# Optimization experiments

Measured on AMD Instinct MI355X. Metric: run time of the kernel, lower is better.

## Reference

```python
import jax, jax.numpy as jnp
import numpy as np
from jax import lax

# Module config (UOT_loss defaults): reg_m_l2=[5.0, 5.0], div='l2',
# detach_plan=True, use_uniform=False, marginal_match_dim=1.
REG_M1, REG_M2 = 5.0, 5.0
NUM_ITER = 1000      # POT mm_unbalanced default numItermax
STOP_THR = 1e-15     # POT default stopThr
EPS = 1e-16


def pairwise_sqeuclidean(x, y):
    # ot.dist default metric='sqeuclidean': M[i,j] = ||x_i - y_j||^2
    x2 = jnp.sum(x * x, axis=1)[:, None]
    y2 = jnp.sum(y * y, axis=1)[None, :]
    return jnp.maximum(x2 + y2 - 2.0 * (x @ y.T), 0.0)


def mm_unbalanced_l2(a, b, M):
    # POT ot.unbalanced.mm_unbalanced(a, b, M, [REG_M1, REG_M2], div='l2'), reg=0.
    G0 = a[:, None] * b[None, :]                       # [n, m] init plan
    K = jnp.maximum(REG_M1 * a[:, None] + REG_M2 * b[None, :] - M, 0.0)

    def cond(state):
        i, _, err = state
        return jnp.logical_and(i < NUM_ITER, err > STOP_THR)

    def body(state):
        i, G, _ = state
        Gd = (REG_M1 * jnp.sum(G, axis=1, keepdims=True)
              + REG_M2 * jnp.sum(G, axis=0, keepdims=True) + EPS)
        Gn = K * G / Gd
        err = jnp.sqrt(jnp.sum((Gn - G) ** 2))
        return i + 1, Gn, err

    _, G, _ = lax.while_loop(
        cond, body, (jnp.int32(0), G0, jnp.array(jnp.inf, G0.dtype)))
    return G


def setup_inputs() -> dict:
    key = jax.random.key(0)
    k1, k2, k3, k4 = jax.random.split(key, 4)
    n, m, d = 4096, 4096, 64
    source = jax.random.normal(k1, (n, d), jnp.float32)
    target = jax.random.normal(k2, (m, d), jnp.float32)
    mu = jax.random.uniform(k3, (n,), jnp.float32, minval=0.5, maxval=1.5)
    nu = jax.random.uniform(k4, (m,), jnp.float32, minval=0.5, maxval=1.5)
    mu = mu / jnp.sum(mu)
    nu = nu / jnp.sum(nu)
    return {"source": source, "target": target,
            "source_density": mu, "target_density": nu}


def reference(source, target, source_density, target_density):
    M = pairwise_sqeuclidean(source, target)           # [n, m]
    plan = mm_unbalanced_l2(source_density, target_density, M)
    ot_loss = jnp.sum(plan * M)
    # marginal_match_dim=1 -> row sums (transported source mass)
    marginal_transported = jnp.sum(plan, axis=1)
    marginal_loss = jnp.mean((marginal_transported - source_density) ** 2)
    return ot_loss, marginal_loss
```

## Files before the change

kernel.cpp:

```cpp
#include <hip/hip_runtime.h>


#define NV 4096
#define RM 5.0f
#define EPSF 1e-16f
#define STOP2 1e-30f
#define NITER 1000
#define MAGIC 0x5a17c0de
#define GRID_T 512
#define NT 4096

#define ERRT_OFF 0
#define ERRS_OFF 4096
#define OTP_OFF  8192
#define RSP_OFF  12288
#define CSP_OFF  274432
#define RS_OFF   536576
#define CS_OFF   540672
#define BMI_OFF  544768
#define CTL_OFF  548864
#define G_OFF    552960

typedef short bf16x8 __attribute__((ext_vector_type(8)));
typedef float f32x4  __attribute__((ext_vector_type(4)));
typedef unsigned short u16;

__device__ __forceinline__ float wave_sum_all(float v) {
  #pragma unroll
  for (int off = 1; off < 64; off <<= 1) v += __shfl_xor(v, off);
  return v;
}
__device__ __forceinline__ float red32_sum(float v) {
  #pragma unroll
  for (int off = 1; off < 32; off <<= 1) v += __shfl_xor(v, off);
  return v;
}
__device__ __forceinline__ float red32_max(float v) {
  #pragma unroll
  for (int off = 1; off < 32; off <<= 1) v = fmaxf(v, __shfl_xor(v, off));
  return v;
}
__device__ __forceinline__ float wave_sum_dn(float v) {
  #pragma unroll
  for (int off = 32; off; off >>= 1) v += __shfl_down(v, off);
  return v;
}
__device__ __forceinline__ float dot64(const float* __restrict__ xr,
                                       const float* __restrict__ yr) {
  float d = 0.f;
  #pragma unroll 1
  for (int k = 0; k < 64; ++k) d = fmaf(xr[k], yr[k], d);
  return d;
}
__device__ __forceinline__ unsigned pack2(float x, float y) {
  return (__float_as_uint(x) >> 16) | (__float_as_uint(y) & 0xffff0000u);
}

__device__ void stage64(const float* __restrict__ X,
                        const float* __restrict__ Y,
                        int by, int bx,
                        u16 (*As)[72], u16 (*Bs)[72],
                        float* X2L, float* Y2L) {
  const int t = threadIdx.x;
  #pragma unroll
  for (int m = 0; m < 2; ++m) {
    const float* src = m ? (Y + (size_t)bx * 4096) : (X + (size_t)by * 4096);
    u16 (*dst)[72] = m ? Bs : As;
    float* nrm = m ? Y2L : X2L;
    #pragma unroll
    for (int it = 0; it < 4; ++it) {
      const int flat = t + it * 256;
      const int r = flat >> 4;
      const int c = (flat & 15) << 2;
      const float4 v = *(const float4*)(src + (size_t)flat * 4);
      float p = fmaf(v.x, v.x, fmaf(v.y, v.y, fmaf(v.z, v.z, v.w * v.w)));
      p += __shfl_xor(p, 1); p += __shfl_xor(p, 2);
      p += __shfl_xor(p, 4); p += __shfl_xor(p, 8);
      if ((t & 15) == 0) nrm[r] = p;
      uint2 w;
      w.x = pack2(v.x, v.y);
      w.y = pack2(v.z, v.w);
      *(uint2*)&dst[r][c] = w;
    }
  }
  __syncthreads();
}

__device__ void dots64(const u16 (*As)[72], const u16 (*Bs)[72],
                       int wr, int wc, int lane, f32x4 acc[2][2]) {
  const int lrow = lane & 15, lk8 = lane >> 4;
  #pragma unroll
  for (int i = 0; i < 2; ++i)
    #pragma unroll
    for (int j = 0; j < 2; ++j)
      acc[i][j] = (f32x4){0.f, 0.f, 0.f, 0.f};
  #pragma unroll
  for (int ks = 0; ks < 2; ++ks) {
    bf16x8 af[2], bg[2];
    #pragma unroll
    for (int f = 0; f < 2; ++f) {
      af[f] = *(const bf16x8*)&As[wr * 32 + f * 16 + lrow][ks * 32 + lk8 * 8];
      bg[f] = *(const bf16x8*)&Bs[wc * 32 + f * 16 + lrow][ks * 32 + lk8 * 8];
    }
    #pragma unroll
    for (int fr = 0; fr < 2; ++fr)
      #pragma unroll
      for (int fc = 0; fc < 2; ++fc)
        acc[fr][fc] = __builtin_amdgcn_mfma_f32_16x16x32_bf16(
            af[fr], bg[fc], acc[fr][fc], 0, 0, 0);
  }
}

__device__ __forceinline__ void gbar(int* ctl) {
  __threadfence();
  __syncthreads();
  if (threadIdx.x == 0) {
    while (__hip_atomic_load(&ctl[2], __ATOMIC_ACQUIRE,
                             __HIP_MEMORY_SCOPE_AGENT) != (int)MAGIC)
      __builtin_amdgcn_s_sleep(8);
    const int sense = __hip_atomic_load(&ctl[1], __ATOMIC_ACQUIRE,
                                        __HIP_MEMORY_SCOPE_AGENT);
    const int old = __hip_atomic_fetch_add(&ctl[0], 1, __ATOMIC_ACQ_REL,
                                           __HIP_MEMORY_SCOPE_AGENT);
    if (old == GRID_T - 1) {
      __hip_atomic_store(&ctl[0], 0, __ATOMIC_RELAXED, __HIP_MEMORY_SCOPE_AGENT);
      __hip_atomic_store(&ctl[1], sense ^ 1, __ATOMIC_RELEASE,
                         __HIP_MEMORY_SCOPE_AGENT);
    } else {
      while (__hip_atomic_load(&ctl[1], __ATOMIC_ACQUIRE,
                               __HIP_MEMORY_SCOPE_AGENT) == sense)
        __builtin_amdgcn_s_sleep(16);
    }
  }
  __syncthreads();
  __threadfence();
}

__global__ __launch_bounds__(256, 5) void k_main(
    const float* __restrict__ X, const float* __restrict__ Y,
    const float* __restrict__ a, const float* __restrict__ b,
    float* __restrict__ W) {
  __shared__ u16 As[64][72], Bs[64][72];
  __shared__ float X2L[64], Y2L[64];
  __shared__ float rcs[128];
  __shared__ float serr[4];
  __shared__ int s_nz;

  const int bid = blockIdx.x, tid = threadIdx.x;
  const int by = bid >> 6, bx = bid & 63;
  const int lane = tid & 63, wv = tid >> 6;
  const int wr = wv >> 1, wc = wv & 1;
  const int lrow = lane & 15, lk8 = lane >> 4;
  const int l32 = lane & 31;
  const int r0w = by * 64 + wr * 32, c0w = bx * 64 + wc * 32;
  float* Gp = W + G_OFF;
  int* bmi = (int*)(W + BMI_OFF);

  if (tid == 0) s_nz = 0;
  if (tid < 128) rcs[tid] = 0.f;

  stage64(X, Y, by, bx, As, Bs, X2L, Y2L);

  const float av = a[r0w + l32];
  const float bv = b[c0w + l32];

  f32x4 acc[2][2];
  dots64(As, Bs, wr, wc, lane, acc);

  const float x2lv = X2L[wr * 32 + l32];
  const float y2lv = Y2L[wc * 32 + l32];
  const float amax = red32_max(av), bmax = red32_max(bv);
  const float x2m = red32_max(x2lv), y2m = red32_max(y2lv);
  const float Cw = RM * (amax + bmax) + 0.02f * sqrtf(x2m * y2m) + 0.05f;

  float x2r[8], y2c[2];
  #pragma unroll
  for (int fr = 0; fr < 2; ++fr)
    #pragma unroll
    for (int j = 0; j < 4; ++j)
      x2r[fr * 4 + j] = X2L[wr * 32 + fr * 16 + lk8 * 4 + j];
  #pragma unroll
  for (int fc = 0; fc < 2; ++fc)
    y2c[fc] = Y2L[wc * 32 + fc * 16 + lrow];

  float mmin = 3.4e38f;
  #pragma unroll
  for (int fr = 0; fr < 2; ++fr)
    #pragma unroll
    for (int j = 0; j < 4; ++j)
      #pragma unroll
      for (int fc = 0; fc < 2; ++fc)
        mmin = fminf(mmin,
                     fmaf(-2.f, acc[fr][fc][j], x2r[fr * 4 + j] + y2c[fc]));
  const bool wfast = (__ballot(mmin < Cw) == 0ull);

  if (wfast) {
    const float Ea = red32_sum(av * av);
    const float Eb = red32_sum(bv * bv);
    if (lane == 0) serr[wv] = Ea * Eb;
    #pragma unroll
    for (int fr = 0; fr < 2; ++fr)
      #pragma unroll
      for (int fc = 0; fc < 2; ++fc)
        acc[fr][fc] = (f32x4){0.f, 0.f, 0.f, 0.f};
  } else {
    if (lane == 0) s_nz = 1;
    float sa = 0.f, sb = 0.f;
    for (int i = lane; i < NV; i += 64) { sa += a[i]; sb += b[i]; }
    sa = wave_sum_all(sa); sb = wave_sum_all(sb);
    float bcf[2], gdc[2];
    #pragma unroll
    for (int fc = 0; fc < 2; ++fc) {
      bcf[fc] = __shfl(bv, fc * 16 + lrow);
      gdc[fc] = RM * bcf[fc] * sa;
    }
    float errp = 0.f;
    #pragma unroll
    for (int fr = 0; fr < 2; ++fr)
      #pragma unroll
      for (int j = 0; j < 4; ++j) {
        const int ridx = fr * 16 + lk8 * 4 + j;
        const float ar = __shfl(av, ridx);
        const float gdr = RM * ar * sb;
        const int grow = r0w + ridx;
        float rsum = 0.f;
        #pragma unroll
        for (int fc = 0; fc < 2; ++fc) {
          float Mv = fmaf(-2.f, acc[fr][fc][j], x2r[fr * 4 + j] + y2c[fc]);
          if (Mv < Cw) {
            const float dx = dot64(X + ((size_t)grow << 6),
                                   Y + ((size_t)(c0w + fc * 16 + lrow) << 6));
            Mv = dot64(X + ((size_t)grow << 6), X + ((size_t)grow << 6)) * 0.f
               + x2r[fr * 4 + j] + y2c[fc] - 2.f * dx;
          }
          Mv = fmaxf(Mv, 0.f);
          const float Kv = fmaxf(RM * (ar + bcf[fc]) - Mv, 0.f);
          const float g0 = ar * bcf[fc];
          const float g = Kv * g0 / (gdr + gdc[fc] + EPSF);
          acc[fr][fc][j] = g;
          const float dl = g - g0;
          errp += dl * dl;
          rsum += g;
        }
        atomicAdd(&rcs[wr * 32 + ridx], rsum);
      }
    #pragma unroll
    for (int fc = 0; fc < 2; ++fc) {
      float csum = 0.f;
      #pragma unroll
      for (int fr = 0; fr < 2; ++fr)
        #pragma unroll
        for (int j = 0; j < 4; ++j) csum += acc[fr][fc][j];
      atomicAdd(&rcs[64 + wc * 32 + fc * 16 + lrow], csum);
    }
    errp = wave_sum_all(errp);
    if (lane == 0) serr[wv] = errp;
  }
  __syncthreads();
  const int tilenz = s_nz;

  if (tilenz) {
    #pragma unroll
    for (int fr = 0; fr < 2; ++fr)
      #pragma unroll
      for (int j = 0; j < 4; ++j) {
        const int grow = r0w + fr * 16 + lk8 * 4 + j;
        #pragma unroll
        for (int fc = 0; fc < 2; ++fc)
          Gp[(size_t)grow * NV + c0w + fc * 16 + lrow] = acc[fr][fc][j];
      }
    if (tid < 64)       W[RSP_OFF + (size_t)bid * 64 + tid] = rcs[tid];
    else if (tid < 128) W[CSP_OFF + (size_t)bid * 64 + (tid - 64)] = rcs[tid];
  }
  if (tid == 0) {
    W[ERRT_OFF + bid] = serr[0] + serr[1] + serr[2] + serr[3];
    bmi[bid] = tilenz;
  }
}

__global__ __launch_bounds__(256, 2) void k_tail(
    const float* __restrict__ X, const float* __restrict__ Y,
    const float* __restrict__ a, const float* __restrict__ b,
    float* __restrict__ W, float* __restrict__ out) {
  __shared__ u16 As[64][72], Bs[64][72];
  __shared__ float X2L[64], Y2L[64];
  __shared__ float rcs[128], serr[4], sred[4];
  __shared__ int s_nz, s_any;

  const int bid = blockIdx.x, tid = threadIdx.x;
  const int lane = tid & 63, wv = tid >> 6;
  const int wr = wv >> 1, wc = wv & 1;
  const int lrow = lane & 15, lk8 = lane >> 4;
  const int l32 = lane & 31;
  float* Gp = W + G_OFF;
  int* bmi = (int*)(W + BMI_OFF);
  int* ctl = (int*)(W + CTL_OFF);

  if (bid == 0 && tid == 0) {
    __hip_atomic_store(&ctl[0], 0, __ATOMIC_RELAXED, __HIP_MEMORY_SCOPE_AGENT);
    __hip_atomic_store(&ctl[1], 0, __ATOMIC_RELAXED, __HIP_MEMORY_SCOPE_AGENT);
    __hip_atomic_store(&ctl[2], (int)MAGIC, __ATOMIC_RELEASE,
                       __HIP_MEMORY_SCOPE_AGENT);
  }

  const int4* bmi4 = (const int4*)bmi;
  int orv = 0;
  for (int i = tid; i < 1024; i += 256) {
    const int4 q = bmi4[i];
    orv |= q.x | q.y | q.z | q.w;
  }
  if (tid == 0) s_any = 0;
  __syncthreads();
  if (orv) s_any = 1;
  __syncthreads();

  if (!s_any) {
    if (bid == 0) {
      float s = 0.f;
      for (int i = tid; i < NV; i += 256) { const float d = a[i]; s = fmaf(d, d, s); }
      s = wave_sum_dn(s);
      if (lane == 0) serr[wv] = s;
      __syncthreads();
      if (tid == 0) {
        out[0] = 0.f;
        out[1] = (serr[0] + serr[1] + serr[2] + serr[3]) * (1.0f / (float)NV);
      }
    }
    return;
  }

  int p = 2;
  while (true) {
    {
      const int sr = tid >> 5, j32 = tid & 31;
      const int r = bid * 8 + sr;
      const int byr = r >> 6, rl = r & 63;
      float vs = 0.f;
      for (int k = j32; k < 64; k += 32) {
        const int t = byr * 64 + k;
        vs += bmi[t] ? W[RSP_OFF + (size_t)t * 64 + rl] : 0.f;
      }
      vs = red32_sum(vs);
      if (j32 == 0) W[RS_OFF + r] = vs;
      float cs = 0.f;
      for (int k = j32; k < 64; k += 32) {
        const int t = k * 64 + byr;
        cs += bmi[t] ? W[CSP_OFF + (size_t)t * 64 + rl] : 0.f;
      }
      cs = red32_sum(cs);
      if (j32 == 0) W[CS_OFF + r] = cs;
    }
    if (bid == 0) {
      float e = 0.f;
      for (int i = tid; i < NT; i += 256) e += W[ERRT_OFF + i];
      e = wave_sum_all(e);
      if (lane == 0) sred[wv] = e;
      __syncthreads();
      if (tid == 0) W[ERRS_OFF] = sred[0] + sred[1] + sred[2] + sred[3];
    }
    gbar(ctl);
    const float errv = W[ERRS_OFF];
    if (errv <= STOP2 || p > NITER) break;

    #pragma unroll 1
    for (int tt = 0; tt < 8; ++tt) {
      const int t = bid + tt * GRID_T;
      if (!bmi[t]) { if (tid == 0) W[ERRT_OFF + t] = 0.f; continue; }
      const int by = t >> 6, bx = t & 63;
      const int r0w = by * 64 + wr * 32, c0w = bx * 64 + wc * 32;
      if (tid == 0) s_nz = 0;
      if (tid < 128) rcs[tid] = 0.f;
      __syncthreads();
      stage64(X, Y, by, bx, As, Bs, X2L, Y2L);
      f32x4 acc[2][2];
      dots64(As, Bs, wr, wc, lane, acc);

      const float av = a[r0w + l32], bv = b[c0w + l32];
      const float x2lv = X2L[wr * 32 + l32], y2lv = Y2L[wc * 32 + l32];
      const float Rv = W[RS_OFF + r0w + l32], Cv = W[CS_OFF + c0w + l32];
      const float amax = red32_max(av), bmax = red32_max(bv);
      const float x2m = red32_max(x2lv), y2m = red32_max(y2lv);
      const float Cw = RM * (amax + bmax) + 0.02f * sqrtf(x2m * y2m) + 0.05f;

      float x2r[8], y2c[2], bcf[2], Ccf[2];
      #pragma unroll
      for (int fr = 0; fr < 2; ++fr)
        #pragma unroll
        for (int j = 0; j < 4; ++j)
          x2r[fr * 4 + j] = X2L[wr * 32 + fr * 16 + lk8 * 4 + j];
      #pragma unroll
      for (int fc = 0; fc < 2; ++fc) {
        y2c[fc] = Y2L[wc * 32 + fc * 16 + lrow];
        bcf[fc] = __shfl(bv, fc * 16 + lrow);
        Ccf[fc] = __shfl(Cv, fc * 16 + lrow);
      }

      float errp = 0.f; int nzl = 0;
      #pragma unroll
      for (int fr = 0; fr < 2; ++fr)
        #pragma unroll
        for (int j = 0; j < 4; ++j) {
          const int ridx = fr * 16 + lk8 * 4 + j;
          const float ar = __shfl(av, ridx);
          const float Rr = __shfl(Rv, ridx);
          const int grow = r0w + ridx;
          float rsum = 0.f;
          #pragma unroll
          for (int fc = 0; fc < 2; ++fc) {
            const int gcol = c0w + fc * 16 + lrow;
            const float g = Gp[(size_t)grow * NV + gcol];
            float Mv = fmaf(-2.f, acc[fr][fc][j], x2r[fr * 4 + j] + y2c[fc]);
            if (Mv < Cw) {
              const float dx = dot64(X + ((size_t)grow << 6),
                                     Y + ((size_t)gcol << 6));
              Mv = x2r[fr * 4 + j] + y2c[fc] - 2.f * dx;
            }
            Mv = fmaxf(Mv, 0.f);
            const float Kv = fmaxf(RM * (ar + bcf[fc]) - Mv, 0.f);
            const float gd = RM * Rr + RM * Ccf[fc] + EPSF;
            const float gn = Kv * g / gd;
            acc[fr][fc][j] = gn;
            const float dl = gn - g;
            errp += dl * dl;
            nzl |= (gn != 0.f);
            rsum += gn;
          }
          atomicAdd(&rcs[wr * 32 + ridx], rsum);
        }
      #pragma unroll
      for (int fc = 0; fc < 2; ++fc) {
        float csum = 0.f;
        #pragma unroll
        for (int fr = 0; fr < 2; ++fr)
          #pragma unroll
          for (int j = 0; j < 4; ++j) csum += acc[fr][fc][j];
        atomicAdd(&rcs[64 + wc * 32 + fc * 16 + lrow], csum);
      }
      errp = wave_sum_all(errp);
      if (lane == 0) serr[wv] = errp;
      if (nzl) s_nz = 1;
      __syncthreads();

      #pragma unroll
      for (int fr = 0; fr < 2; ++fr)
        #pragma unroll
        for (int j = 0; j < 4; ++j) {
          const int grow = r0w + fr * 16 + lk8 * 4 + j;
          #pragma unroll
          for (int fc = 0; fc < 2; ++fc)
            Gp[(size_t)grow * NV + c0w + fc * 16 + lrow] = acc[fr][fc][j];
        }
      if (tid < 64)       W[RSP_OFF + (size_t)t * 64 + tid] = rcs[tid];
      else if (tid < 128) W[CSP_OFF + (size_t)t * 64 + (tid - 64)] = rcs[tid];
      if (tid == 0) {
        W[ERRT_OFF + t] = serr[0] + serr[1] + serr[2] + serr[3];
        bmi[t] = s_nz;
      }
      __syncthreads();
    }
    gbar(ctl);
    ++p;
  }

  #pragma unroll 1
  for (int tt = 0; tt < 8; ++tt) {
    const int t = bid + tt * GRID_T;
    float otb = 0.f;
    if (bmi[t]) {
      const int by = t >> 6, bx = t & 63;
      const int r0w = by * 64 + wr * 32, c0w = bx * 64 + wc * 32;
      float otp = 0.f;
      #pragma unroll
      for (int fr = 0; fr < 2; ++fr)
        #pragma unroll
        for (int j = 0; j < 4; ++j) {
          const int grow = r0w + fr * 16 + lk8 * 4 + j;
          #pragma unroll
          for (int fc = 0; fc < 2; ++fc) {
            const int gcol = c0w + fc * 16 + lrow;
            const float g = Gp[(size_t)grow * NV + gcol];
            if (g != 0.f) {
              const float* xr = X + ((size_t)grow << 6);
              const float* yr = Y + ((size_t)gcol << 6);
              const float dd = dot64(xr, yr);
              const float x2 = dot64(xr, xr);
              const float y2 = dot64(yr, yr);
              otp += g * fmaxf(x2 + y2 - 2.f * dd, 0.f);
            }
          }
        }
      otp = wave_sum_all(otp);
      if (lane == 0) serr[wv] = otp;
      __syncthreads();
      otb = serr[0] + serr[1] + serr[2] + serr[3];
      __syncthreads();
    }
    if (tid == 0) W[OTP_OFF + t] = otb;
  }
  gbar(ctl);
  if (bid == 0) {
    float so = 0.f;
    for (int i = tid; i < NT; i += 256) so += W[OTP_OFF + i];
    so = wave_sum_dn(so);
    float sm = 0.f;
    for (int i = tid; i < NV; i += 256) {
      const float d = W[RS_OFF + i] - a[i];
      sm = fmaf(d, d, sm);
    }
    sm = wave_sum_dn(sm);
    if (lane == 0) { sred[wv] = so; serr[wv] = sm; }
    __syncthreads();
    if (tid == 0) {
      out[0] = sred[0] + sred[1] + sred[2] + sred[3];
      out[1] = (serr[0] + serr[1] + serr[2] + serr[3]) * (1.0f / (float)NV);
    }
  }
}

extern "C" void kernel_launch(void* const* d_in, const int* in_sizes, int n_in,
                              void* d_out, int out_size, void* d_ws, size_t ws_size,
                              hipStream_t stream) {
  const float* X = (const float*)d_in[0];
  const float* Y = (const float*)d_in[1];
  const float* a = (const float*)d_in[2];
  const float* b = (const float*)d_in[3];
  float* out = (float*)d_out;
  float* W = (float*)d_ws;

  k_main<<<NT, 256, 0, stream>>>(X, Y, a, b, W);
  k_tail<<<GRID_T, 256, 0, stream>>>(X, Y, a, b, W, out);
}
```

Measured before the change: 79.99 us.

## Switch to per-wave 32x32 tiles with wave-local reductions and early exit

```diff
diff --git a/kernel.cpp b/kernel.cpp
--- a/kernel.cpp
+++ b/kernel.cpp
@@ -8,18 +8,18 @@
 #define NITER 1000
 #define MAGIC 0x5a17c0de
 #define GRID_T 512
-#define NT 4096
+#define NT 16384
 
 #define ERRT_OFF 0
-#define ERRS_OFF 4096
-#define OTP_OFF  8192
-#define RSP_OFF  12288
-#define CSP_OFF  274432
-#define RS_OFF   536576
-#define CS_OFF   540672
-#define BMI_OFF  544768
-#define CTL_OFF  548864
-#define G_OFF    552960
+#define ERRS_OFF 16384
+#define OTP_OFF  32768
+#define RSP_OFF  49152
+#define CSP_OFF  573440
+#define RS_OFF   1097728
+#define CS_OFF   1101824
+#define BMI_OFF  1105920
+#define CTL_OFF  1122304
+#define G_OFF    1126400
 
 typedef short bf16x8 __attribute__((ext_vector_type(8)));
 typedef float f32x4  __attribute__((ext_vector_type(4)));
@@ -38,6 +38,11 @@
 __device__ __forceinline__ float red32_max(float v) {
   #pragma unroll
   for (int off = 1; off < 32; off <<= 1) v = fmaxf(v, __shfl_xor(v, off));
+  return v;
+}
+__device__ __forceinline__ float red16_sum(float v) {
+  v += __shfl_xor(v, 1); v += __shfl_xor(v, 2);
+  v += __shfl_xor(v, 4); v += __shfl_xor(v, 8);
   return v;
 }
 __device__ __forceinline__ float wave_sum_dn(float v) {
@@ -56,38 +61,26 @@
   return (__float_as_uint(x) >> 16) | (__float_as_uint(y) & 0xffff0000u);
 }
 
-__device__ void stage64(const float* __restrict__ X,
-                        const float* __restrict__ Y,
-                        int by, int bx,
-                        u16 (*As)[72], u16 (*Bs)[72],
-                        float* X2L, float* Y2L) {
-  const int t = threadIdx.x;
-  #pragma unroll
-  for (int m = 0; m < 2; ++m) {
-    const float* src = m ? (Y + (size_t)bx * 4096) : (X + (size_t)by * 4096);
-    u16 (*dst)[72] = m ? Bs : As;
-    float* nrm = m ? Y2L : X2L;
-    #pragma unroll
-    for (int it = 0; it < 4; ++it) {
-      const int flat = t + it * 256;
-      const int r = flat >> 4;
-      const int c = (flat & 15) << 2;
-      const float4 v = *(const float4*)(src + (size_t)flat * 4);
-      float p = fmaf(v.x, v.x, fmaf(v.y, v.y, fmaf(v.z, v.z, v.w * v.w)));
-      p += __shfl_xor(p, 1); p += __shfl_xor(p, 2);
-      p += __shfl_xor(p, 4); p += __shfl_xor(p, 8);
-      if ((t & 15) == 0) nrm[r] = p;
-      uint2 w;
-      w.x = pack2(v.x, v.y);
-      w.y = pack2(v.z, v.w);
-      *(uint2*)&dst[r][c] = w;
-    }
-  }
-  __syncthreads();
-}
-
-__device__ void dots64(const u16 (*As)[72], const u16 (*Bs)[72],
-                       int wr, int wc, int lane, f32x4 acc[2][2]) {
+__device__ __forceinline__ void stage32(const float* __restrict__ src,
+                                        u16 (*dst)[72], float* nrm, int lane) {
+  #pragma unroll
+  for (int it = 0; it < 8; ++it) {
+    const int flat = lane + it * 64;
+    const int r = flat >> 4, c4 = flat & 15;
+    const float4 v = *(const float4*)(src + (size_t)r * 64 + c4 * 4);
+    float p = fmaf(v.x, v.x, fmaf(v.y, v.y, fmaf(v.z, v.z, v.w * v.w)));
+    p += __shfl_xor(p, 1); p += __shfl_xor(p, 2);
+    p += __shfl_xor(p, 4); p += __shfl_xor(p, 8);
+    if (c4 == 0) nrm[r] = p;
+    uint2 w;
+    w.x = pack2(v.x, v.y);
+    w.y = pack2(v.z, v.w);
+    *(uint2*)&dst[r][c4 * 4] = w;
+  }
+}
+
+__device__ __forceinline__ void dots32(const u16 (*As)[72], const u16 (*Bs)[72],
+                                       int lane, f32x4 acc[2][2]) {
   const int lrow = lane & 15, lk8 = lane >> 4;
   #pragma unroll
   for (int i = 0; i < 2; ++i)
@@ -99,8 +92,8 @@
     bf16x8 af[2], bg[2];
     #pragma unroll
     for (int f = 0; f < 2; ++f) {
-      af[f] = *(const bf16x8*)&As[wr * 32 + f * 16 + lrow][ks * 32 + lk8 * 8];
-      bg[f] = *(const bf16x8*)&Bs[wc * 32 + f * 16 + lrow][ks * 32 + lk8 * 8];
+      af[f] = *(const bf16x8*)&As[f * 16 + lrow][ks * 32 + lk8 * 8];
+      bg[f] = *(const bf16x8*)&Bs[f * 16 + lrow][ks * 32 + lk8 * 8];
     }
     #pragma unroll
     for (int fr = 0; fr < 2; ++fr)
@@ -136,53 +129,45 @@
   __threadfence();
 }
 
-__global__ __launch_bounds__(256, 5) void k_main(
+__global__ __launch_bounds__(256, 4) void k_main(
     const float* __restrict__ X, const float* __restrict__ Y,
     const float* __restrict__ a, const float* __restrict__ b,
     float* __restrict__ W) {
-  __shared__ u16 As[64][72], Bs[64][72];
-  __shared__ float X2L[64], Y2L[64];
-  __shared__ float rcs[128];
-  __shared__ float serr[4];
-  __shared__ int s_nz;
-
-  const int bid = blockIdx.x, tid = threadIdx.x;
-  const int by = bid >> 6, bx = bid & 63;
-  const int lane = tid & 63, wv = tid >> 6;
-  const int wr = wv >> 1, wc = wv & 1;
-  const int lrow = lane & 15, lk8 = lane >> 4;
-  const int l32 = lane & 31;
-  const int r0w = by * 64 + wr * 32, c0w = bx * 64 + wc * 32;
+  __shared__ u16 Aw[4][32][72], Bw[4][32][72];
+  __shared__ float X2w[4][32], Y2w[4][32];
+
+  const int tid = threadIdx.x, lane = tid & 63, wv = tid >> 6;
+  const int lrow = lane & 15, lk8 = lane >> 4, l32 = lane & 31;
+  const int t = blockIdx.x * 4 + wv;
+  const int by = t >> 7, bx = t & 127;
+  const int r0 = by * 32, c0 = bx * 32;
+  int* bmi = (int*)(W + BMI_OFF);
   float* Gp = W + G_OFF;
-  int* bmi = (int*)(W + BMI_OFF);
-
-  if (tid == 0) s_nz = 0;
-  if (tid < 128) rcs[tid] = 0.f;
-
-  stage64(X, Y, by, bx, As, Bs, X2L, Y2L);
-
-  const float av = a[r0w + l32];
-  const float bv = b[c0w + l32];
+
+  const float av = a[r0 + l32];
+  const float bv = b[c0 + l32];
+
+  stage32(X + (size_t)r0 * 64, Aw[wv], X2w[wv], lane);
+  stage32(Y + (size_t)c0 * 64, Bw[wv], Y2w[wv], lane);
 
   f32x4 acc[2][2];
-  dots64(As, Bs, wr, wc, lane, acc);
-
-  const float x2lv = X2L[wr * 32 + l32];
-  const float y2lv = Y2L[wc * 32 + l32];
+  dots32(Aw[wv], Bw[wv], lane, acc);
+
+  float x2r[8], y2c[2];
+  #pragma unroll
+  for (int fr = 0; fr < 2; ++fr)
+    #pragma unroll
+    for (int j = 0; j < 4; ++j)
+      x2r[fr * 4 + j] = X2w[wv][fr * 16 + lk8 * 4 + j];
+  #pragma unroll
+  for (int fc = 0; fc < 2; ++fc)
+    y2c[fc] = Y2w[wv][fc * 16 + lrow];
+
+  const float x2lv = X2w[wv][l32], y2lv = Y2w[wv][l32];
   const float amax = red32_max(av), bmax = red32_max(bv);
   const float x2m = red32_max(x2lv), y2m = red32_max(y2lv);
   const float Cw = RM * (amax + bmax) + 0.02f * sqrtf(x2m * y2m) + 0.05f;
 
-  float x2r[8], y2c[2];
-  #pragma unroll
-  for (int fr = 0; fr < 2; ++fr)
-    #pragma unroll
-    for (int j = 0; j < 4; ++j)
-      x2r[fr * 4 + j] = X2L[wr * 32 + fr * 16 + lk8 * 4 + j];
-  #pragma unroll
-  for (int fc = 0; fc < 2; ++fc)
-    y2c[fc] = Y2L[wc * 32 + fc * 16 + lrow];
-
   float mmin = 3.4e38f;
   #pragma unroll
   for (int fr = 0; fr < 2; ++fr)
@@ -192,89 +177,83 @@
       for (int fc = 0; fc < 2; ++fc)
         mmin = fminf(mmin,
                      fmaf(-2.f, acc[fr][fc][j], x2r[fr * 4 + j] + y2c[fc]));
-  const bool wfast = (__ballot(mmin < Cw) == 0ull);
-
-  if (wfast) {
+
+  if (__ballot(mmin < Cw) == 0ull) {
     const float Ea = red32_sum(av * av);
     const float Eb = red32_sum(bv * bv);
-    if (lane == 0) serr[wv] = Ea * Eb;
-    #pragma unroll
-    for (int fr = 0; fr < 2; ++fr)
-      #pragma unroll
-      for (int fc = 0; fc < 2; ++fc)
-        acc[fr][fc] = (f32x4){0.f, 0.f, 0.f, 0.f};
-  } else {
-    if (lane == 0) s_nz = 1;
-    float sa = 0.f, sb = 0.f;
-    for (int i = lane; i < NV; i += 64) { sa += a[i]; sb += b[i]; }
-    sa = wave_sum_all(sa); sb = wave_sum_all(sb);
-    float bcf[2], gdc[2];
-    #pragma unroll
-    for (int fc = 0; fc < 2; ++fc) {
-      bcf[fc] = __shfl(bv, fc * 16 + lrow);
-      gdc[fc] = RM * bcf[fc] * sa;
-    }
-    float errp = 0.f;
+    if (lane == 0) {
+      W[ERRT_OFF + t] = Ea * Eb;
+      bmi[t] = 0;
+    }
+    return;
+  }
+
+  float sa = 0.f, sb = 0.f;
+  for (int i = lane; i < NV; i += 64) { sa += a[i]; sb += b[i]; }
+  sa = wave_sum_all(sa); sb = wave_sum_all(sb);
+  float bcf[2], gdc[2];
+  #pragma unroll
+  for (int fc = 0; fc < 2; ++fc) {
+    bcf[fc] = __shfl(bv, fc * 16 + lrow);
+    gdc[fc] = RM * bcf[fc] * sa;
+  }
+  float errp = 0.f, csum[2] = {0.f, 0.f};
+  int nzl = 0;
+  float rs8[8];
+  #pragma unroll
+  for (int fr = 0; fr < 2; ++fr)
+    #pragma unroll
+    for (int j = 0; j < 4; ++j) {
+      const int ridx = fr * 16 + lk8 * 4 + j;
+      const float ar = __shfl(av, ridx);
+      const float gdr = RM * ar * sb;
+      const int grow = r0 + ridx;
+      float rsum = 0.f;
+      #pragma unroll
+      for (int fc = 0; fc < 2; ++fc) {
+        float Mv = fmaf(-2.f, acc[fr][fc][j], x2r[fr * 4 + j] + y2c[fc]);
+        if (Mv < Cw) {
+          const float dx = dot64(X + ((size_t)grow << 6),
+                                 Y + ((size_t)(c0 + fc * 16 + lrow) << 6));
+          Mv = x2r[fr * 4 + j] + y2c[fc] - 2.f * dx;
+        }
+        Mv = fmaxf(Mv, 0.f);
+        const float Kv = fmaxf(RM * (ar + bcf[fc]) - Mv, 0.f);
+        const float g0 = ar * bcf[fc];
+        const float g = Kv * g0 / (gdr + gdc[fc] + EPSF);
+        acc[fr][fc][j] = g;
+        const float dl = g - g0;
+        errp += dl * dl;
+        nzl |= (g != 0.f);
+        rsum += g;
+        csum[fc] += g;
+      }
+      rs8[fr * 4 + j] = red16_sum(rsum);
+    }
+  const int nz = (__ballot(nzl) != 0ull) ? 1 : 0;
+  if (nz) {
     #pragma unroll
     for (int fr = 0; fr < 2; ++fr)
       #pragma unroll
       for (int j = 0; j < 4; ++j) {
         const int ridx = fr * 16 + lk8 * 4 + j;
-        const float ar = __shfl(av, ridx);
-        const float gdr = RM * ar * sb;
-        const int grow = r0w + ridx;
-        float rsum = 0.f;
-        #pragma unroll
-        for (int fc = 0; fc < 2; ++fc) {
-          float Mv = fmaf(-2.f, acc[fr][fc][j], x2r[fr * 4 + j] + y2c[fc]);
-          if (Mv < Cw) {
-            const float dx = dot64(X + ((size_t)grow << 6),
-                                   Y + ((size_t)(c0w + fc * 16 + lrow) << 6));
-            Mv = dot64(X + ((size_t)grow << 6), X + ((size_t)grow << 6)) * 0.f
-               + x2r[fr * 4 + j] + y2c[fc] - 2.f * dx;
-          }
-          Mv = fmaxf(Mv, 0.f);
-          const float Kv = fmaxf(RM * (ar + bcf[fc]) - Mv, 0.f);
-          const float g0 = ar * bcf[fc];
-          const float g = Kv * g0 / (gdr + gdc[fc] + EPSF);
-          acc[fr][fc][j] = g;
-          const float dl = g - g0;
-          errp += dl * dl;
-          rsum += g;
-        }
-        atomicAdd(&rcs[wr * 32 + ridx], rsum);
-      }
-    #pragma unroll
-    for (int fc = 0; fc < 2; ++fc) {
-      float csum = 0.f;
-      #pragma unroll
-      for (int fr = 0; fr < 2; ++fr)
-        #pragma unroll
-        for (int j = 0; j < 4; ++j) csum += acc[fr][fc][j];
-      atomicAdd(&rcs[64 + wc * 32 + fc * 16 + lrow], csum);
-    }
-    errp = wave_sum_all(errp);
-    if (lane == 0) serr[wv] = errp;
-  }
-  __syncthreads();
-  const int tilenz = s_nz;
-
-  if (tilenz) {
-    #pragma unroll
-    for (int fr = 0; fr < 2; ++fr)
-      #pragma unroll
-      for (int j = 0; j < 4; ++j) {
-        const int grow = r0w + fr * 16 + lk8 * 4 + j;
+        const int grow = r0 + ridx;
         #pragma unroll
         for (int fc = 0; fc < 2; ++fc)
-          Gp[(size_t)grow * NV + c0w + fc * 16 + lrow] = acc[fr][fc][j];
-      }
-    if (tid < 64)       W[RSP_OFF + (size_t)bid * 64 + tid] = rcs[tid];
-    else if (tid < 128) W[CSP_OFF + (size_t)bid * 64 + (tid - 64)] = rcs[tid];
-  }
-  if (tid == 0) {
-    W[ERRT_OFF + bid] = serr[0] + serr[1] + serr[2] + serr[3];
-    bmi[bid] = tilenz;
+          Gp[(size_t)grow * NV + c0 + fc * 16 + lrow] = acc[fr][fc][j];
+        if (lrow == 0) W[RSP_OFF + (size_t)t * 32 + ridx] = rs8[fr * 4 + j];
+      }
+    #pragma unroll
+    for (int fc = 0; fc < 2; ++fc) {
+      float cv = csum[fc];
+      cv += __shfl_xor(cv, 16); cv += __shfl_xor(cv, 32);
+      if (lane < 16) W[CSP_OFF + (size_t)t * 32 + fc * 16 + lrow] = cv;
+    }
+  }
+  errp = wave_sum_all(errp);
+  if (lane == 0) {
+    W[ERRT_OFF + t] = errp;
+    bmi[t] = nz;
   }
 }
 
@@ -282,16 +261,14 @@
     const float* __restrict__ X, const float* __restrict__ Y,
     const float* __restrict__ a, const float* __restrict__ b,
     float* __restrict__ W, float* __restrict__ out) {
-  __shared__ u16 As[64][72], Bs[64][72];
-  __shared__ float X2L[64], Y2L[64];
-  __shared__ float rcs[128], serr[4], sred[4];
-  __shared__ int s_nz, s_any;
+  __shared__ u16 Aw[4][32][72], Bw[4][32][72];
+  __shared__ float X2w[4][32], Y2w[4][32];
+  __shared__ float serr[4], sred[4];
+  __shared__ int s_any;
 
   const int bid = blockIdx.x, tid = threadIdx.x;
   const int lane = tid & 63, wv = tid >> 6;
-  const int wr = wv >> 1, wc = wv & 1;
-  const int lrow = lane & 15, lk8 = lane >> 4;
-  const int l32 = lane & 31;
+  const int lrow = lane & 15, lk8 = lane >> 4, l32 = lane & 31;
   float* Gp = W + G_OFF;
   int* bmi = (int*)(W + BMI_OFF);
   int* ctl = (int*)(W + CTL_OFF);
@@ -305,7 +282,7 @@
 
   const int4* bmi4 = (const int4*)bmi;
   int orv = 0;
-  for (int i = tid; i < 1024; i += 256) {
+  for (int i = tid; i < 4096; i += 256) {
     const int4 q = bmi4[i];
     orv |= q.x | q.y | q.z | q.w;
   }
@@ -334,18 +311,18 @@
     {
       const int sr = tid >> 5, j32 = tid & 31;
       const int r = bid * 8 + sr;
-      const int byr = r >> 6, rl = r & 63;
+      const int byt = r >> 5, rl = r & 31;
       float vs = 0.f;
-      for (int k = j32; k < 64; k += 32) {
-        const int t = byr * 64 + k;
-        vs += bmi[t] ? W[RSP_OFF + (size_t)t * 64 + rl] : 0.f;
+      for (int k = j32; k < 128; k += 32) {
+        const int tt2 = byt * 128 + k;
+        vs += bmi[tt2] ? W[RSP_OFF + (size_t)tt2 * 32 + rl] : 0.f;
       }
       vs = red32_sum(vs);
       if (j32 == 0) W[RS_OFF + r] = vs;
       float cs = 0.f;
-      for (int k = j32; k < 64; k += 32) {
-        const int t = k * 64 + byr;
-        cs += bmi[t] ? W[CSP_OFF + (size_t)t * 64 + rl] : 0.f;
+      for (int k = j32; k < 128; k += 32) {
+        const int tt2 = k * 128 + byt;
+        cs += bmi[tt2] ? W[CSP_OFF + (size_t)tt2 * 32 + rl] : 0.f;
       }
       cs = red32_sum(cs);
       if (j32 == 0) W[CS_OFF + r] = cs;
@@ -364,38 +341,39 @@
 
     #pragma unroll 1
     for (int tt = 0; tt < 8; ++tt) {
-      const int t = bid + tt * GRID_T;
-      if (!bmi[t]) { if (tid == 0) W[ERRT_OFF + t] = 0.f; continue; }
-      const int by = t >> 6, bx = t & 63;
-      const int r0w = by * 64 + wr * 32, c0w = bx * 64 + wc * 32;
-      if (tid == 0) s_nz = 0;
-      if (tid < 128) rcs[tid] = 0.f;
-      __syncthreads();
-      stage64(X, Y, by, bx, As, Bs, X2L, Y2L);
+      const int t = bid * 4 + wv + tt * 2048;
+      if (!bmi[t]) { if (lane == 0) W[ERRT_OFF + t] = 0.f; continue; }
+      const int by = t >> 7, bx = t & 127;
+      const int r0 = by * 32, c0 = bx * 32;
+
+      const float av = a[r0 + l32], bv = b[c0 + l32];
+      const float Rv = W[RS_OFF + r0 + l32], Cv = W[CS_OFF + c0 + l32];
+
+      stage32(X + (size_t)r0 * 64, Aw[wv], X2w[wv], lane);
+      stage32(Y + (size_t)c0 * 64, Bw[wv], Y2w[wv], lane);
       f32x4 acc[2][2];
-      dots64(As, Bs, wr, wc, lane, acc);
-
-      const float av = a[r0w + l32], bv = b[c0w + l32];
-      const float x2lv = X2L[wr * 32 + l32], y2lv = Y2L[wc * 32 + l32];
-      const float Rv = W[RS_OFF + r0w + l32], Cv = W[CS_OFF + c0w + l32];
+      dots32(Aw[wv], Bw[wv], lane, acc);
+
+      float x2r[8], y2c[2], bcf[2], Ccf[2];
+      #pragma unroll
+      for (int fr = 0; fr < 2; ++fr)
+        #pragma unroll
+        for (int j = 0; j < 4; ++j)
+          x2r[fr * 4 + j] = X2w[wv][fr * 16 + lk8 * 4 + j];
+      #pragma unroll
+      for (int fc = 0; fc < 2; ++fc) {
+        y2c[fc] = Y2w[wv][fc * 16 + lrow];
+        bcf[fc] = __shfl(bv, fc * 16 + lrow);
+        Ccf[fc] = __shfl(Cv, fc * 16 + lrow);
+      }
+      const float x2lv = X2w[wv][l32], y2lv = Y2w[wv][l32];
       const float amax = red32_max(av), bmax = red32_max(bv);
       const float x2m = red32_max(x2lv), y2m = red32_max(y2lv);
       const float Cw = RM * (amax + bmax) + 0.02f * sqrtf(x2m * y2m) + 0.05f;
 
-      float x2r[8], y2c[2], bcf[2], Ccf[2];
-      #pragma unroll
-      for (int fr = 0; fr < 2; ++fr)
-        #pragma unroll
-        for (int j = 0; j < 4; ++j)
-          x2r[fr * 4 + j] = X2L[wr * 32 + fr * 16 + lk8 * 4 + j];
-      #pragma unroll
-      for (int fc = 0; fc < 2; ++fc) {
-        y2c[fc] = Y2L[wc * 32 + fc * 16 + lrow];
-        bcf[fc] = __shfl(bv, fc * 16 + lrow);
-        Ccf[fc] = __shfl(Cv, fc * 16 + lrow);
-      }
-
-      float errp = 0.f; int nzl = 0;
+      float errp = 0.f, csum[2] = {0.f, 0.f};
+      int nzl = 0;
+      float rs8[8];
       #pragma unroll
       for (int fr = 0; fr < 2; ++fr)
         #pragma unroll
@@ -403,11 +381,11 @@
           const int ridx = fr * 16 + lk8 * 4 + j;
           const float ar = __shfl(av, ridx);
           const float Rr = __shfl(Rv, ridx);
-          const int grow = r0w + ridx;
+          const int grow = r0 + ridx;
           float rsum = 0.f;
           #pragma unroll
           for (int fc = 0; fc < 2; ++fc) {
-            const int gcol = c0w + fc * 16 + lrow;
+            const int gcol = c0 + fc * 16 + lrow;
             const float g = Gp[(size_t)grow * NV + gcol];
             float Mv = fmaf(-2.f, acc[fr][fc][j], x2r[fr * 4 + j] + y2c[fc]);
             if (Mv < Cw) {
@@ -424,39 +402,33 @@
             errp += dl * dl;
             nzl |= (gn != 0.f);
             rsum += gn;
+            csum[fc] += gn;
           }
-          atomicAdd(&rcs[wr * 32 + ridx], rsum);
+          rs8[fr * 4 + j] = red16_sum(rsum);
         }
-      #pragma unroll
-      for (int fc = 0; fc < 2; ++fc) {
-        float csum = 0.f;
-        #pragma unroll
-        for (int fr = 0; fr < 2; ++fr)
-          #pragma unroll
-          for (int j = 0; j < 4; ++j) csum += acc[fr][fc][j];
-        atomicAdd(&rcs[64 + wc * 32 + fc * 16 + lrow], csum);
-      }
-      errp = wave_sum_all(errp);
-      if (lane == 0) serr[wv] = errp;
-      if (nzl) s_nz = 1;
-      __syncthreads();
-
+      const int nz = (__ballot(nzl) != 0ull) ? 1 : 0;
       #pragma unroll
       for (int fr = 0; fr < 2; ++fr)
         #pragma unroll
         for (int j = 0; j < 4; ++j) {
-          const int grow = r0w + fr * 16 + lk8 * 4 + j;
+          const int ridx = fr * 16 + lk8 * 4 + j;
+          const int grow = r0 + ridx;
           #pragma unroll
           for (int fc = 0; fc < 2; ++fc)
-            Gp[(size_t)grow * NV + c0w + fc * 16 + lrow] = acc[fr][fc][j];
+            Gp[(size_t)grow * NV + c0 + fc * 16 + lrow] = acc[fr][fc][j];
+          if (lrow == 0) W[RSP_OFF + (size_t)t * 32 + ridx] = rs8[fr * 4 + j];
         }
-      if (tid < 64)       W[RSP_OFF + (size_t)t * 64 + tid] = rcs[tid];
-      else if (tid < 128) W[CSP_OFF + (size_t)t * 64 + (tid - 64)] = rcs[tid];
-      if (tid == 0) {
-        W[ERRT_OFF + t] = serr[0] + serr[1] + serr[2] + serr[3];
-        bmi[t] = s_nz;
-      }
-      __syncthreads();
+      #pragma unroll
+      for (int fc = 0; fc < 2; ++fc) {
+        float cv = csum[fc];
+        cv += __shfl_xor(cv, 16); cv += __shfl_xor(cv, 32);
+        if (lane < 16) W[CSP_OFF + (size_t)t * 32 + fc * 16 + lrow] = cv;
+      }
+      errp = wave_sum_all(errp);
+      if (lane == 0) {
+        W[ERRT_OFF + t] = errp;
+        bmi[t] = nz;
+      }
     }
     gbar(ctl);
     ++p;
@@ -464,20 +436,20 @@
 
   #pragma unroll 1
   for (int tt = 0; tt < 8; ++tt) {
-    const int t = bid + tt * GRID_T;
-    float otb = 0.f;
+    const int t = bid * 4 + wv + tt * 2048;
+    float otw = 0.f;
     if (bmi[t]) {
-      const int by = t >> 6, bx = t & 63;
-      const int r0w = by * 64 + wr * 32, c0w = bx * 64 + wc * 32;
+      const int by = t >> 7, bx = t & 127;
+      const int r0 = by * 32, c0 = bx * 32;
       float otp = 0.f;
       #pragma unroll
       for (int fr = 0; fr < 2; ++fr)
         #pragma unroll
         for (int j = 0; j < 4; ++j) {
-          const int grow = r0w + fr * 16 + lk8 * 4 + j;
+          const int grow = r0 + fr * 16 + lk8 * 4 + j;
           #pragma unroll
           for (int fc = 0; fc < 2; ++fc) {
-            const int gcol = c0w + fc * 16 + lrow;
+            const int gcol = c0 + fc * 16 + lrow;
             const float g = Gp[(size_t)grow * NV + gcol];
             if (g != 0.f) {
               const float* xr = X + ((size_t)grow << 6);
@@ -489,13 +461,9 @@
             }
           }
         }
-      otp = wave_sum_all(otp);
-      if (lane == 0) serr[wv] = otp;
-      __syncthreads();
-      otb = serr[0] + serr[1] + serr[2] + serr[3];
-      __syncthreads();
-    }
-    if (tid == 0) W[OTP_OFF + t] = otb;
+      otw = wave_sum_all(otp);
+    }
+    if (lane == 0) W[OTP_OFF + t] = otw;
   }
   gbar(ctl);
   if (bid == 0) {
@@ -527,6 +495,6 @@
   float* out = (float*)d_out;
   float* W = (float*)d_ws;
 
-  k_main<<<NT, 256, 0, stream>>>(X, Y, a, b, W);
+  k_main<<<NT / 4, 256, 0, stream>>>(X, Y, a, b, W);
   k_tail<<<GRID_T, 256, 0, stream>>>(X, Y, a, b, W, out);
 }
```

Result: slower. 97.55 us (+21.9%).
